# Performance work log

Measured on AMD Instinct MI355X. Metric: run time of the kernel, lower is better.

The kernel has to match this reference:

```python
import jax, jax.numpy as jnp
import numpy as np

D_MODEL = 1024
N_HEAD = 16

def setup_inputs() -> dict:
    key = jax.random.key(0)
    ks = jax.random.split(key, 11)
    B, S, D = 2, 2048, D_MODEL
    s = 1.0 / np.sqrt(D)
    inp = {
        'q': jax.random.normal(ks[0], (B, S, D), jnp.float32),
        'k': jax.random.normal(ks[1], (B, S, D), jnp.float32),
        'v': jax.random.normal(ks[2], (B, S, D), jnp.float32),
        'w_q': jax.random.normal(ks[3], (D, D), jnp.float32) * s,
        'b_q': jnp.zeros((D,), jnp.float32),
        'w_k': jax.random.normal(ks[4], (D, D), jnp.float32) * s,
        'b_k': jnp.zeros((D,), jnp.float32),
        'w_v': jax.random.normal(ks[5], (D, D), jnp.float32) * s,
        'b_v': jnp.zeros((D,), jnp.float32),
        'w_o': jax.random.normal(ks[6], (D, D), jnp.float32) * s,
        'b_o': jnp.zeros((D,), jnp.float32),
    }
    return inp

def _split_heads(x):
    B, S, D = x.shape
    return x.reshape(B, S, N_HEAD, D // N_HEAD).transpose(0, 2, 1, 3)  # [B,H,S,d]

def reference(q, k, v, w_q, b_q, w_k, b_k, w_v, b_v, w_o, b_o):
    # Linear projections (torch Linear: x @ W.T + b)
    qh = _split_heads(q @ w_q.T + b_q)
    kh = _split_heads(k @ w_k.T + b_k)
    vh = _split_heads(v @ w_v.T + b_v)
    d_k = qh.shape[-1]
    scores = jnp.einsum('bhqd,bhkd->bhqk', qh, kh) / jnp.sqrt(jnp.float32(d_k))
    attn = jax.nn.softmax(scores, axis=-1)
    out = jnp.einsum('bhqk,bhkd->bhqd', attn, vh)  # [B,H,S,d]
    B, H, S, d = out.shape
    out = out.transpose(0, 2, 1, 3).reshape(B, S, H * d)
    return out @ w_o.T + b_o
```

## Files before the change

### kernel.cpp

```cpp
#include <hip/hip_runtime.h>
#include <hip/hip_bf16.h>

typedef __hip_bfloat16 bf16;
typedef short bf16x8 __attribute__((ext_vector_type(8)));
typedef float f32x4 __attribute__((ext_vector_type(4)));

#define D_MODEL 1024
#define SEQ     2048
#define NHEAD   16
#define DHEAD   64
#define BATCH   2
#define MROWS   (BATCH*SEQ)
#define LOG2E   1.4426950408889634f

__device__ __forceinline__ void lds_dma16(const bf16* g, bf16* l) {
  __builtin_amdgcn_global_load_lds(
      (const __attribute__((address_space(1))) void*)g,
      (__attribute__((address_space(3))) void*)l, 16, 0, 0);
}

__device__ __forceinline__ uint4 pack8_f32(const float4 x0, const float4 x1) {
  union { uint4 q; bf16 h[8]; } pk;
  pk.h[0]=__float2bfloat16(x0.x); pk.h[1]=__float2bfloat16(x0.y);
  pk.h[2]=__float2bfloat16(x0.z); pk.h[3]=__float2bfloat16(x0.w);
  pk.h[4]=__float2bfloat16(x1.x); pk.h[5]=__float2bfloat16(x1.y);
  pk.h[6]=__float2bfloat16(x1.z); pk.h[7]=__float2bfloat16(x1.w);
  return pk.q;
}

__global__ __launch_bounds__(256) void convert7(
    const float* s0, const float* s1, const float* s2, const float* s3,
    const float* s4, const float* s5, const float* s6,
    bf16* d0, bf16* d1, bf16* d2, bf16* d3, bf16* d4, bf16* d5, bf16* d6)
{
  const float* S[7] = {s0,s1,s2,s3,s4,s5,s6};
  bf16*        D[7] = {d0,d1,d2,d3,d4,d5,d6};
  const int z = blockIdx.y;
  const int n8 = (z < 3) ? (MROWS*D_MODEL/8) : (D_MODEL*D_MODEL/8);
  for (int i = blockIdx.x*256 + threadIdx.x; i < n8; i += 512*256) {
    float4 a = ((const float4*)S[z])[2*i];
    float4 b = ((const float4*)S[z])[2*i+1];
    ((uint4*)D[z])[i] = pack8_f32(a, b);
  }
}

__global__ __launch_bounds__(256) void gemm3_dma(
    const bf16* A0, const bf16* A1, const bf16* A2,
    const bf16* W0, const bf16* W1, const bf16* W2,
    const float* B0, const float* B1, const float* B2,
    bf16* C0, bf16* C1, bf16* VpT)
{
  __shared__ __align__(16) bf16 As[8*128*8];
  __shared__ __align__(16) bf16 Ws[8*128*8];
  const int z = blockIdx.z;
  const bf16* A = (z == 0) ? A0 : (z == 1) ? A1 : A2;
  const bf16* W = (z == 0) ? W0 : (z == 1) ? W1 : W2;
  const float* Bv = (z == 0) ? B0 : (z == 1) ? B1 : B2;
  const int K = D_MODEL, N = D_MODEL;
  const int tid  = threadIdx.x;
  const int lane = tid & 63, wave = tid >> 6;
  const int wm   = wave >> 1, wn = wave & 1;
  const int quad = lane >> 4, l16 = lane & 15;
  const int row0 = blockIdx.y * 128, col0 = blockIdx.x * 128;

  const f32x4 zero = {0.f, 0.f, 0.f, 0.f};
  f32x4 acc[4][4];
  #pragma unroll
  for (int i = 0; i < 4; ++i)
    #pragma unroll
    for (int j = 0; j < 4; ++j) acc[i][j] = zero;

  for (int k0 = 0; k0 < K; k0 += 64) {
    __syncthreads();
    #pragma unroll
    for (int t = 0; t < 4; ++t) {
      int s = t*256 + tid;
      int g = s >> 7, r = s & 127;
      lds_dma16(A + (size_t)(row0 + r)*K + k0 + g*8, &As[s*8]);
      lds_dma16(W + (size_t)(col0 + r)*K + k0 + g*8, &Ws[s*8]);
    }
    __syncthreads();
    #pragma unroll
    for (int ks = 0; ks < 2; ++ks) {
      bf16x8 af[4], wf[4];
      #pragma unroll
      for (int mt = 0; mt < 4; ++mt)
        af[mt] = *(const bf16x8*)&As[((ks*4 + quad)*128 + wm*64 + mt*16 + l16)*8];
      #pragma unroll
      for (int nt = 0; nt < 4; ++nt)
        wf[nt] = *(const bf16x8*)&Ws[((ks*4 + quad)*128 + wn*64 + nt*16 + l16)*8];
      #pragma unroll
      for (int mt = 0; mt < 4; ++mt)
        #pragma unroll
        for (int nt = 0; nt < 4; ++nt)
          acc[mt][nt] = __builtin_amdgcn_mfma_f32_16x16x32_bf16(af[mt], wf[nt], acc[mt][nt], 0, 0, 0);
    }
  }

  if (z < 2) {
    bf16* C = (z == 0) ? C0 : C1;
    const float scale = (z == 0) ? 0.125f*LOG2E : 1.0f;
    #pragma unroll
    for (int nt = 0; nt < 4; ++nt) {
      int c = col0 + wn*64 + nt*16 + l16;
      float bv = Bv[c];
      #pragma unroll
      for (int mt = 0; mt < 4; ++mt) {
        int r = row0 + wm*64 + mt*16 + quad*4;
        #pragma unroll
        for (int j = 0; j < 4; ++j)
          C[(size_t)(r + j)*N + c] = __float2bfloat16((acc[mt][nt][j] + bv) * scale);
      }
    }
  } else {
    const int bb = row0 >> 11;
    const int sbase = (row0 & 2047) + wm*64;
    #pragma unroll
    for (int nt = 0; nt < 4; ++nt) {
      int c = col0 + wn*64 + nt*16 + l16;
      float bv = Bv[c];
      bf16* col = VpT + (size_t)((bb << 10) + c) * SEQ;
      #pragma unroll
      for (int mt = 0; mt < 4; ++mt) {
        int s = sbase + mt*16 + quad*4;
        union { uint2 u; bf16 h[4]; } pk;
        #pragma unroll
        for (int j = 0; j < 4; ++j) pk.h[j] = __float2bfloat16(acc[mt][nt][j] + bv);
        *(uint2*)(col + s) = pk.u;
      }
    }
  }
}

__global__ __launch_bounds__(256) void gemm_out_dma(
    const bf16* __restrict__ A, const bf16* __restrict__ W,
    const float* __restrict__ Bv, float* __restrict__ C)
{
  __shared__ __align__(16) bf16 As[8*128*8];
  __shared__ __align__(16) bf16 Ws[8*64*8];
  const int K = D_MODEL, N = D_MODEL;
  const int tid  = threadIdx.x;
  const int lane = tid & 63, wave = tid >> 6;
  const int wm   = wave >> 1, wn = wave & 1;
  const int quad = lane >> 4, l16 = lane & 15;
  const int row0 = blockIdx.y * 128, col0 = blockIdx.x * 64;

  const f32x4 zero = {0.f, 0.f, 0.f, 0.f};
  f32x4 acc[4][2];
  #pragma unroll
  for (int i = 0; i < 4; ++i)
    #pragma unroll
    for (int j = 0; j < 2; ++j) acc[i][j] = zero;

  for (int k0 = 0; k0 < K; k0 += 64) {
    __syncthreads();
    #pragma unroll
    for (int t = 0; t < 4; ++t) {
      int s = t*256 + tid;
      int g = s >> 7, r = s & 127;
      lds_dma16(A + (size_t)(row0 + r)*K + k0 + g*8, &As[s*8]);
    }
    #pragma unroll
    for (int t = 0; t < 2; ++t) {
      int s = t*256 + tid;
      int g = s >> 6, r = s & 63;
      lds_dma16(W + (size_t)(col0 + r)*K + k0 + g*8, &Ws[s*8]);
    }
    __syncthreads();
    #pragma unroll
    for (int ks = 0; ks < 2; ++ks) {
      bf16x8 af[4], wf[2];
      #pragma unroll
      for (int mt = 0; mt < 4; ++mt)
        af[mt] = *(const bf16x8*)&As[((ks*4 + quad)*128 + wm*64 + mt*16 + l16)*8];
      #pragma unroll
      for (int nt = 0; nt < 2; ++nt)
        wf[nt] = *(const bf16x8*)&Ws[((ks*4 + quad)*64 + wn*32 + nt*16 + l16)*8];
      #pragma unroll
      for (int mt = 0; mt < 4; ++mt)
        #pragma unroll
        for (int nt = 0; nt < 2; ++nt)
          acc[mt][nt] = __builtin_amdgcn_mfma_f32_16x16x32_bf16(af[mt], wf[nt], acc[mt][nt], 0, 0, 0);
    }
  }

  #pragma unroll
  for (int nt = 0; nt < 2; ++nt) {
    int c = col0 + wn*32 + nt*16 + l16;
    float bv = Bv[c];
    #pragma unroll
    for (int mt = 0; mt < 4; ++mt) {
      int r = row0 + wm*64 + mt*16 + quad*4;
      #pragma unroll
      for (int j = 0; j < 4; ++j)
        C[(size_t)(r + j)*N + c] = acc[mt][nt][j] + bv;
    }
  }
}

__global__ __launch_bounds__(256) void gemm3_fused(
    const float* A0, const float* A1, const float* A2,
    const float* W0, const float* W1, const float* W2,
    const float* B0, const float* B1, const float* B2,
    bf16* C0, bf16* C1, bf16* VpT)
{
  __shared__ __align__(16) bf16 As[4*128*8];
  __shared__ __align__(16) bf16 Ws[4*128*8];
  const int z = blockIdx.z;
  const float* A = (z == 0) ? A0 : (z == 1) ? A1 : A2;
  const float* W = (z == 0) ? W0 : (z == 1) ? W1 : W2;
  const float* Bv = (z == 0) ? B0 : (z == 1) ? B1 : B2;
  const int K = D_MODEL, N = D_MODEL;
  const int tid  = threadIdx.x;
  const int lane = tid & 63, wave = tid >> 6;
  const int wm   = wave >> 1, wn = wave & 1;
  const int quad = lane >> 4, l16 = lane & 15;
  const int row0 = blockIdx.y * 128, col0 = blockIdx.x * 128;

  const f32x4 zero = {0.f, 0.f, 0.f, 0.f};
  f32x4 acc[4][4];
  #pragma unroll
  for (int i = 0; i < 4; ++i)
    #pragma unroll
    for (int j = 0; j < 4; ++j) acc[i][j] = zero;

  for (int k0 = 0; k0 < K; k0 += 32) {
    __syncthreads();
    #pragma unroll
    for (int t = 0; t < 2; ++t) {
      int s = t*256 + tid;
      int g = s >> 7, r = s & 127;
      const float* Af = A + (size_t)(row0 + r)*K + k0 + g*8;
      *(uint4*)&As[s*8] = pack8_f32(((const float4*)Af)[0], ((const float4*)Af)[1]);
      const float* Wf = W + (size_t)(col0 + r)*K + k0 + g*8;
      *(uint4*)&Ws[s*8] = pack8_f32(((const float4*)Wf)[0], ((const float4*)Wf)[1]);
    }
    __syncthreads();
    bf16x8 af[4], wf[4];
    #pragma unroll
    for (int mt = 0; mt < 4; ++mt)
      af[mt] = *(const bf16x8*)&As[(quad*128 + wm*64 + mt*16 + l16)*8];
    #pragma unroll
    for (int nt = 0; nt < 4; ++nt)
      wf[nt] = *(const bf16x8*)&Ws[(quad*128 + wn*64 + nt*16 + l16)*8];
    #pragma unroll
    for (int mt = 0; mt < 4; ++mt)
      #pragma unroll
      for (int nt = 0; nt < 4; ++nt)
        acc[mt][nt] = __builtin_amdgcn_mfma_f32_16x16x32_bf16(af[mt], wf[nt], acc[mt][nt], 0, 0, 0);
  }

  if (z < 2) {
    bf16* C = (z == 0) ? C0 : C1;
    const float scale = (z == 0) ? 0.125f*LOG2E : 1.0f;
    #pragma unroll
    for (int nt = 0; nt < 4; ++nt) {
      int c = col0 + wn*64 + nt*16 + l16;
      float bv = Bv[c];
      #pragma unroll
      for (int mt = 0; mt < 4; ++mt) {
        int r = row0 + wm*64 + mt*16 + quad*4;
        #pragma unroll
        for (int j = 0; j < 4; ++j)
          C[(size_t)(r + j)*N + c] = __float2bfloat16((acc[mt][nt][j] + bv) * scale);
      }
    }
  } else {
    const int bb = row0 >> 11;
    const int sbase = (row0 & 2047) + wm*64;
    #pragma unroll
    for (int nt = 0; nt < 4; ++nt) {
      int c = col0 + wn*64 + nt*16 + l16;
      float bv = Bv[c];
      bf16* col = VpT + (size_t)((bb << 10) + c) * SEQ;
      #pragma unroll
      for (int mt = 0; mt < 4; ++mt) {
        int s = sbase + mt*16 + quad*4;
        union { uint2 u; bf16 h[4]; } pk;
        #pragma unroll
        for (int j = 0; j < 4; ++j) pk.h[j] = __float2bfloat16(acc[mt][nt][j] + bv);
        *(uint2*)(col + s) = pk.u;
      }
    }
  }
}

__global__ __launch_bounds__(256) void gemm_out_fused(
    const bf16* __restrict__ A, const float* __restrict__ W,
    const float* __restrict__ Bv, float* __restrict__ C)
{
  __shared__ __align__(16) bf16 As[4*128*8];
  __shared__ __align__(16) bf16 Ws[4*64*8];
  const int K = D_MODEL, N = D_MODEL;
  const int tid  = threadIdx.x;
  const int lane = tid & 63, wave = tid >> 6;
  const int wm   = wave >> 1, wn = wave & 1;
  const int quad = lane >> 4, l16 = lane & 15;
  const int row0 = blockIdx.y * 128, col0 = blockIdx.x * 64;

  const f32x4 zero = {0.f, 0.f, 0.f, 0.f};
  f32x4 acc[4][2];
  #pragma unroll
  for (int i = 0; i < 4; ++i)
    #pragma unroll
    for (int j = 0; j < 2; ++j) acc[i][j] = zero;

  for (int k0 = 0; k0 < K; k0 += 32) {
    __syncthreads();
    #pragma unroll
    for (int t = 0; t < 2; ++t) {
      int s = t*256 + tid;
      int g = s >> 7, r = s & 127;
      *(uint4*)&As[s*8] = *(const uint4*)(A + (size_t)(row0 + r)*K + k0 + g*8);
    }
    {
      int g = tid >> 6, r = tid & 63;
      const float* Wf = W + (size_t)(col0 + r)*K + k0 + g*8;
      *(uint4*)&Ws[tid*8] = pack8_f32(((const float4*)Wf)[0], ((const float4*)Wf)[1]);
    }
    __syncthreads();
    bf16x8 af[4], wf[2];
    #pragma unroll
    for (int mt = 0; mt < 4; ++mt)
      af[mt] = *(const bf16x8*)&As[(quad*128 + wm*64 + mt*16 + l16)*8];
    #pragma unroll
    for (int nt = 0; nt < 2; ++nt)
      wf[nt] = *(const bf16x8*)&Ws[(quad*64 + wn*32 + nt*16 + l16)*8];
    #pragma unroll
    for (int mt = 0; mt < 4; ++mt)
      #pragma unroll
      for (int nt = 0; nt < 2; ++nt)
        acc[mt][nt] = __builtin_amdgcn_mfma_f32_16x16x32_bf16(af[mt], wf[nt], acc[mt][nt], 0, 0, 0);
  }
  #pragma unroll
  for (int nt = 0; nt < 2; ++nt) {
    int c = col0 + wn*32 + nt*16 + l16;
    float bv = Bv[c];
    #pragma unroll
    for (int mt = 0; mt < 4; ++mt) {
      int r = row0 + wm*64 + mt*16 + quad*4;
      #pragma unroll
      for (int j = 0; j < 4; ++j)
        C[(size_t)(r + j)*N + c] = acc[mt][nt][j] + bv;
    }
  }
}

__global__ __launch_bounds__(512) void attn_fused(
    const bf16* __restrict__ Qp, const bf16* __restrict__ Kp,
    const bf16* __restrict__ VpT, bf16* __restrict__ Ao)
{
  __shared__ __align__(16) bf16 UN[128*128];
  __shared__ __align__(16) bf16 Ks[8*128*8];
  __shared__ __align__(16) bf16 Vt[64*16*8];

  const int tid  = threadIdx.x;
  const int lane = tid & 63, wave = tid >> 6;
  const int quad = lane >> 4, l16 = lane & 15;
  const int qt = blockIdx.x, h = blockIdx.y, b = blockIdx.z;
  const int q0 = qt * 128;
  const bf16* Qb = Qp + ((size_t)b*SEQ + q0)*D_MODEL + h*DHEAD;
  const bf16* Kb = Kp + (size_t)b*SEQ*D_MODEL + h*DHEAD;
  const bf16* Vg = VpT + (size_t)((b << 10) + h*DHEAD) * SEQ;

  #pragma unroll
  for (int t = 0; t < 2; ++t) {
    int s = t*512 + tid;
    int g = s >> 7, r = s & 127;
    lds_dma16(Qb + (size_t)r*D_MODEL + g*8, &UN[s*8]);
  }
  __syncthreads();

  const int wq0 = wave * 16;
  const int q   = wq0 + l16;
  bf16x8 qa[2];
  #pragma unroll
  for (int ks = 0; ks < 2; ++ks)
    qa[ks] = *(const bf16x8*)&UN[((ks*4 + quad)*128 + q)*8];
  __syncthreads();
  bf16* Ps = UN;
  const int swz = (l16 & 7) << 1;

  const f32x4 zero = {0.f, 0.f, 0.f, 0.f};
  f32x4 acc_o[4];
  #pragma unroll
  for (int dt = 0; dt < 4; ++dt) acc_o[dt] = zero;
  float m_s = -1e30f, l_s = 0.f;

  for (int kt = 0; kt < SEQ/128; ++kt) {
    #pragma unroll
    for (int t = 0; t < 2; ++t) {
      int s = t*512 + tid;
      int g = s >> 7, kk = s & 127;
      lds_dma16(Kb + (size_t)(kt*128 + kk)*D_MODEL + g*8, &Ks[s*8]);
    }
    #pragma unroll
    for (int t = 0; t < 2; ++t) {
      int c = t*512 + tid;
      int n = c >> 4, gk = c & 15;
      uint4 raw = *(const uint4*)(Vg + (size_t)n*SEQ + kt*128 + gk*8);
      int sw = (gk + n + (n >> 3)) & 15;
      *(uint4*)&Vt[(n*16 + sw)*8] = raw;
    }
    __syncthreads();

    f32x4 sc[8];
    #pragma unroll
    for (int kt2 = 0; kt2 < 8; ++kt2) sc[kt2] = zero;
    #pragma unroll
    for (int ks = 0; ks < 2; ++ks) {
      bf16x8 kf[8];
      #pragma unroll
      for (int kt2 = 0; kt2 < 8; ++kt2)
        kf[kt2] = *(const bf16x8*)&Ks[((ks*4 + quad)*128 + kt2*16 + l16)*8];
      #pragma unroll
      for (int kt2 = 0; kt2 < 8; ++kt2)
        sc[kt2] = __builtin_amdgcn_mfma_f32_16x16x32_bf16(kf[kt2], qa[ks], sc[kt2], 0, 0, 0);
    }

    float vmax = -1e30f;
    #pragma unroll
    for (int kt2 = 0; kt2 < 8; ++kt2) {
      f32x4 s4 = sc[kt2];
      vmax = fmaxf(vmax, fmaxf(fmaxf(s4[0], s4[1]), fmaxf(s4[2], s4[3])));
    }
    vmax = fmaxf(vmax, __shfl_xor(vmax, 16));
    vmax = fmaxf(vmax, __shfl_xor(vmax, 32));
    float mnew  = fmaxf(m_s, vmax);
    float alpha = __builtin_amdgcn_exp2f(m_s - mnew);
    float rs = 0.f;
    #pragma unroll
    for (int kt2 = 0; kt2 < 8; ++kt2) {
      float p0 = __builtin_amdgcn_exp2f(sc[kt2][0] - mnew);
      float p1 = __builtin_amdgcn_exp2f(sc[kt2][1] - mnew);
      float p2 = __builtin_amdgcn_exp2f(sc[kt2][2] - mnew);
      float p3 = __builtin_amdgcn_exp2f(sc[kt2][3] - mnew);
      rs += (p0 + p1) + (p2 + p3);
      union { uint2 u; bf16 hh[4]; } pk;
      pk.hh[0] = __float2bfloat16(p0); pk.hh[1] = __float2bfloat16(p1);
      pk.hh[2] = __float2bfloat16(p2); pk.hh[3] = __float2bfloat16(p3);
      int phys = (kt2*4 + quad) ^ swz;
      *(uint2*)&Ps[q*128 + phys*4] = pk.u;
    }
    rs += __shfl_xor(rs, 16);
    rs += __shfl_xor(rs, 32);
    l_s = l_s*alpha + rs;
    m_s = mnew;
    #pragma unroll
    for (int dt = 0; dt < 4; ++dt) acc_o[dt] = acc_o[dt] * alpha;

    #pragma unroll
    for (int ks2 = 0; ks2 < 4; ++ks2) {
      bf16x8 vf[4], pa;
      #pragma unroll
      for (int dt = 0; dt < 4; ++dt) {
        int n = dt*16 + l16;
        int sw = (ks2*4 + quad + n + (n >> 3)) & 15;
        vf[dt] = *(const bf16x8*)&Vt[(n*16 + sw)*8];
      }
      int phys = (ks2*8 + quad*2) ^ swz;
      pa = *(const bf16x8*)&Ps[q*128 + phys*4];
      #pragma unroll
      for (int dt = 0; dt < 4; ++dt)
        acc_o[dt] = __builtin_amdgcn_mfma_f32_16x16x32_bf16(vf[dt], pa, acc_o[dt], 0, 0, 0);
    }
    __syncthreads();
  }

  bf16* Ob = Ao + ((size_t)b*SEQ + q0)*D_MODEL + h*DHEAD;
  float inv = 1.f / l_s;
  #pragma unroll
  for (int dt = 0; dt < 4; ++dt) {
    union { uint2 u; bf16 hh[4]; } pk;
    #pragma unroll
    for (int j = 0; j < 4; ++j) pk.hh[j] = __float2bfloat16(acc_o[dt][j] * inv);
    *(uint2*)(Ob + (size_t)q*D_MODEL + dt*16 + quad*4) = pk.u;
  }
}

extern "C" void kernel_launch(void* const* d_in, const int* in_sizes, int n_in,
                              void* d_out, int out_size, void* d_ws, size_t ws_size,
                              hipStream_t stream) {
  const float* q   = (const float*)d_in[0];
  const float* k   = (const float*)d_in[1];
  const float* v   = (const float*)d_in[2];
  const float* w_q = (const float*)d_in[3];
  const float* b_q = (const float*)d_in[4];
  const float* w_k = (const float*)d_in[5];
  const float* b_k = (const float*)d_in[6];
  const float* w_v = (const float*)d_in[7];
  const float* b_v = (const float*)d_in[8];
  const float* w_o = (const float*)d_in[9];
  const float* b_o = (const float*)d_in[10];

  const size_t nbuf = (size_t)MROWS * D_MODEL;
  const size_t wbuf = (size_t)D_MODEL * D_MODEL;
  bf16* Kp  = (bf16*)d_out;
  bf16* VpT = Kp + nbuf;

  const size_t needA = 256 + (3*nbuf + 4*wbuf + nbuf) * 2;
  if (ws_size >= needA) {
    bf16* qc  = (bf16*)((char*)d_ws + 256);
    bf16* kc  = qc  + nbuf;
    bf16* vc  = kc  + nbuf;
    bf16* wqc = vc  + nbuf;
    bf16* wkc = wqc + wbuf;
    bf16* wvc = wkc + wbuf;
    bf16* woc = wvc + wbuf;
    bf16* Qp  = woc + wbuf;
    bf16* Ao  = Qp;

    convert7<<<dim3(512,7), 256, 0, stream>>>(q, k, v, w_q, w_k, w_v, w_o,
                                              qc, kc, vc, wqc, wkc, wvc, woc);
    gemm3_dma<<<dim3(8,32,3), 256, 0, stream>>>(qc, kc, vc, wqc, wkc, wvc,
                                                b_q, b_k, b_v, Qp, Kp, VpT);
    attn_fused<<<dim3(16,16,2), 512, 0, stream>>>(Qp, Kp, VpT, Ao);
    gemm_out_dma<<<dim3(16,32), 256, 0, stream>>>(Ao, woc, b_o, (float*)d_out);
  } else {
    bf16* Qp = (bf16*)((char*)d_ws + 256);
    bf16* Ao = Qp;
    gemm3_fused<<<dim3(8,32,3), 256, 0, stream>>>(q, k, v, w_q, w_k, w_v,
                                                  b_q, b_k, b_v, Qp, Kp, VpT);
    attn_fused<<<dim3(16,16,2), 512, 0, stream>>>(Qp, Kp, VpT, Ao);
    gemm_out_fused<<<dim3(16,32), 256, 0, stream>>>(Ao, w_o, b_o, (float*)d_out);
  }
}
```

Before: 309.7 us.

## Swap MFMA operands for vectorized GEMM stores and prefetch V tiles in attention

In the projection GEMMs, the MFMA operands are swapped so each lane holds four consecutive output columns. This lets the epilogue write packed 8-byte bf16 or 16-byte float4 stores and read the bias with float4 loads, instead of scalar strided stores. In the attention kernel, the V-transpose tile for the next iteration is loaded from global memory into registers one step ahead, and the end-of-loop barrier moves to the top of the loop. This hides global load latency behind compute, at the cost of extra registers and an altered synchronization pattern.

```diff
diff --git a/kernel.cpp b/kernel.cpp
--- a/kernel.cpp
+++ b/kernel.cpp
@@ -56,6 +56,7 @@
   const bf16* A = (z == 0) ? A0 : (z == 1) ? A1 : A2;
   const bf16* W = (z == 0) ? W0 : (z == 1) ? W1 : W2;
   const float* Bv = (z == 0) ? B0 : (z == 1) ? B1 : B2;
+  const bool swapped = (z < 2);
   const int K = D_MODEL, N = D_MODEL;
   const int tid  = threadIdx.x;
   const int lane = tid & 63, wave = tid >> 6;
@@ -89,27 +90,38 @@
       #pragma unroll
       for (int nt = 0; nt < 4; ++nt)
         wf[nt] = *(const bf16x8*)&Ws[((ks*4 + quad)*128 + wn*64 + nt*16 + l16)*8];
-      #pragma unroll
-      for (int mt = 0; mt < 4; ++mt)
-        #pragma unroll
-        for (int nt = 0; nt < 4; ++nt)
-          acc[mt][nt] = __builtin_amdgcn_mfma_f32_16x16x32_bf16(af[mt], wf[nt], acc[mt][nt], 0, 0, 0);
-    }
-  }
-
-  if (z < 2) {
+      if (swapped) {
+        #pragma unroll
+        for (int mt = 0; mt < 4; ++mt)
+          #pragma unroll
+          for (int nt = 0; nt < 4; ++nt)
+            acc[mt][nt] = __builtin_amdgcn_mfma_f32_16x16x32_bf16(wf[nt], af[mt], acc[mt][nt], 0, 0, 0);
+      } else {
+        #pragma unroll
+        for (int mt = 0; mt < 4; ++mt)
+          #pragma unroll
+          for (int nt = 0; nt < 4; ++nt)
+            acc[mt][nt] = __builtin_amdgcn_mfma_f32_16x16x32_bf16(af[mt], wf[nt], acc[mt][nt], 0, 0, 0);
+      }
+    }
+  }
+
+  if (swapped) {
     bf16* C = (z == 0) ? C0 : C1;
     const float scale = (z == 0) ? 0.125f*LOG2E : 1.0f;
     #pragma unroll
-    for (int nt = 0; nt < 4; ++nt) {
-      int c = col0 + wn*64 + nt*16 + l16;
-      float bv = Bv[c];
-      #pragma unroll
-      for (int mt = 0; mt < 4; ++mt) {
-        int r = row0 + wm*64 + mt*16 + quad*4;
-        #pragma unroll
-        for (int j = 0; j < 4; ++j)
-          C[(size_t)(r + j)*N + c] = __float2bfloat16((acc[mt][nt][j] + bv) * scale);
+    for (int mt = 0; mt < 4; ++mt) {
+      int r = row0 + wm*64 + mt*16 + l16;
+      #pragma unroll
+      for (int nt = 0; nt < 4; ++nt) {
+        int c0 = col0 + wn*64 + nt*16 + quad*4;
+        float4 b4 = *(const float4*)(Bv + c0);
+        union { uint2 u; bf16 h[4]; } pk;
+        pk.h[0] = __float2bfloat16((acc[mt][nt][0] + b4.x) * scale);
+        pk.h[1] = __float2bfloat16((acc[mt][nt][1] + b4.y) * scale);
+        pk.h[2] = __float2bfloat16((acc[mt][nt][2] + b4.z) * scale);
+        pk.h[3] = __float2bfloat16((acc[mt][nt][3] + b4.w) * scale);
+        *(uint2*)&C[(size_t)r*N + c0] = pk.u;
       }
     }
   } else {
@@ -180,20 +192,21 @@
       for (int mt = 0; mt < 4; ++mt)
         #pragma unroll
         for (int nt = 0; nt < 2; ++nt)
-          acc[mt][nt] = __builtin_amdgcn_mfma_f32_16x16x32_bf16(af[mt], wf[nt], acc[mt][nt], 0, 0, 0);
-    }
-  }
-
-  #pragma unroll
-  for (int nt = 0; nt < 2; ++nt) {
-    int c = col0 + wn*32 + nt*16 + l16;
-    float bv = Bv[c];
-    #pragma unroll
-    for (int mt = 0; mt < 4; ++mt) {
-      int r = row0 + wm*64 + mt*16 + quad*4;
-      #pragma unroll
-      for (int j = 0; j < 4; ++j)
-        C[(size_t)(r + j)*N + c] = acc[mt][nt][j] + bv;
+          acc[mt][nt] = __builtin_amdgcn_mfma_f32_16x16x32_bf16(wf[nt], af[mt], acc[mt][nt], 0, 0, 0);
+    }
+  }
+
+  #pragma unroll
+  for (int mt = 0; mt < 4; ++mt) {
+    int r = row0 + wm*64 + mt*16 + l16;
+    #pragma unroll
+    for (int nt = 0; nt < 2; ++nt) {
+      int c0 = col0 + wn*32 + nt*16 + quad*4;
+      float4 b4 = *(const float4*)(Bv + c0);
+      float4 o;
+      o.x = acc[mt][nt][0] + b4.x; o.y = acc[mt][nt][1] + b4.y;
+      o.z = acc[mt][nt][2] + b4.z; o.w = acc[mt][nt][3] + b4.w;
+      *(float4*)&C[(size_t)r*N + c0] = o;
     }
   }
 }
@@ -210,6 +223,7 @@
   const float* A = (z == 0) ? A0 : (z == 1) ? A1 : A2;
   const float* W = (z == 0) ? W0 : (z == 1) ? W1 : W2;
   const float* Bv = (z == 0) ? B0 : (z == 1) ? B1 : B2;
+  const bool swapped = (z < 2);
   const int K = D_MODEL, N = D_MODEL;
   const int tid  = threadIdx.x;
   const int lane = tid & 63, wave = tid >> 6;
@@ -243,26 +257,37 @@
     #pragma unroll
     for (int nt = 0; nt < 4; ++nt)
       wf[nt] = *(const bf16x8*)&Ws[(quad*128 + wn*64 + nt*16 + l16)*8];
-    #pragma unroll
-    for (int mt = 0; mt < 4; ++mt)
-      #pragma unroll
-      for (int nt = 0; nt < 4; ++nt)
-        acc[mt][nt] = __builtin_amdgcn_mfma_f32_16x16x32_bf16(af[mt], wf[nt], acc[mt][nt], 0, 0, 0);
-  }
-
-  if (z < 2) {
+    if (swapped) {
+      #pragma unroll
+      for (int mt = 0; mt < 4; ++mt)
+        #pragma unroll
+        for (int nt = 0; nt < 4; ++nt)
+          acc[mt][nt] = __builtin_amdgcn_mfma_f32_16x16x32_bf16(wf[nt], af[mt], acc[mt][nt], 0, 0, 0);
+    } else {
+      #pragma unroll
+      for (int mt = 0; mt < 4; ++mt)
+        #pragma unroll
+        for (int nt = 0; nt < 4; ++nt)
+          acc[mt][nt] = __builtin_amdgcn_mfma_f32_16x16x32_bf16(af[mt], wf[nt], acc[mt][nt], 0, 0, 0);
+    }
+  }
+
+  if (swapped) {
     bf16* C = (z == 0) ? C0 : C1;
     const float scale = (z == 0) ? 0.125f*LOG2E : 1.0f;
     #pragma unroll
-    for (int nt = 0; nt < 4; ++nt) {
-      int c = col0 + wn*64 + nt*16 + l16;
-      float bv = Bv[c];
-      #pragma unroll
-      for (int mt = 0; mt < 4; ++mt) {
-        int r = row0 + wm*64 + mt*16 + quad*4;
-        #pragma unroll
-        for (int j = 0; j < 4; ++j)
-          C[(size_t)(r + j)*N + c] = __float2bfloat16((acc[mt][nt][j] + bv) * scale);
+    for (int mt = 0; mt < 4; ++mt) {
+      int r = row0 + wm*64 + mt*16 + l16;
+      #pragma unroll
+      for (int nt = 0; nt < 4; ++nt) {
+        int c0 = col0 + wn*64 + nt*16 + quad*4;
+        float4 b4 = *(const float4*)(Bv + c0);
+        union { uint2 u; bf16 h[4]; } pk;
+        pk.h[0] = __float2bfloat16((acc[mt][nt][0] + b4.x) * scale);
+        pk.h[1] = __float2bfloat16((acc[mt][nt][1] + b4.y) * scale);
+        pk.h[2] = __float2bfloat16((acc[mt][nt][2] + b4.z) * scale);
+        pk.h[3] = __float2bfloat16((acc[mt][nt][3] + b4.w) * scale);
+        *(uint2*)&C[(size_t)r*N + c0] = pk.u;
       }
     }
   } else {
@@ -330,18 +355,19 @@
     for (int mt = 0; mt < 4; ++mt)
       #pragma unroll
       for (int nt = 0; nt < 2; ++nt)
-        acc[mt][nt] = __builtin_amdgcn_mfma_f32_16x16x32_bf16(af[mt], wf[nt], acc[mt][nt], 0, 0, 0);
-  }
-  #pragma unroll
-  for (int nt = 0; nt < 2; ++nt) {
-    int c = col0 + wn*32 + nt*16 + l16;
-    float bv = Bv[c];
-    #pragma unroll
-    for (int mt = 0; mt < 4; ++mt) {
-      int r = row0 + wm*64 + mt*16 + quad*4;
-      #pragma unroll
-      for (int j = 0; j < 4; ++j)
-        C[(size_t)(r + j)*N + c] = acc[mt][nt][j] + bv;
+        acc[mt][nt] = __builtin_amdgcn_mfma_f32_16x16x32_bf16(wf[nt], af[mt], acc[mt][nt], 0, 0, 0);
+  }
+  #pragma unroll
+  for (int mt = 0; mt < 4; ++mt) {
+    int r = row0 + wm*64 + mt*16 + l16;
+    #pragma unroll
+    for (int nt = 0; nt < 2; ++nt) {
+      int c0 = col0 + wn*32 + nt*16 + quad*4;
+      float4 b4 = *(const float4*)(Bv + c0);
+      float4 o;
+      o.x = acc[mt][nt][0] + b4.x; o.y = acc[mt][nt][1] + b4.y;
+      o.z = acc[mt][nt][2] + b4.z; o.w = acc[mt][nt][3] + b4.w;
+      *(float4*)&C[(size_t)r*N + c0] = o;
     }
   }
 }
@@ -377,10 +403,16 @@
   #pragma unroll
   for (int ks = 0; ks < 2; ++ks)
     qa[ks] = *(const bf16x8*)&UN[((ks*4 + quad)*128 + q)*8];
-  __syncthreads();
   bf16* Ps = UN;
   const int swz = (l16 & 7) << 1;
 
+  const int vn0 = tid >> 4,        vgk0 = tid & 15;
+  const int vn1 = (512+tid) >> 4,  vgk1 = (512+tid) & 15;
+  const int vsw0 = (vgk0 + vn0 + (vn0 >> 3)) & 15;
+  const int vsw1 = (vgk1 + vn1 + (vn1 >> 3)) & 15;
+  uint4 vreg0 = *(const uint4*)(Vg + (size_t)vn0*SEQ + vgk0*8);
+  uint4 vreg1 = *(const uint4*)(Vg + (size_t)vn1*SEQ + vgk1*8);
+
   const f32x4 zero = {0.f, 0.f, 0.f, 0.f};
   f32x4 acc_o[4];
   #pragma unroll
@@ -388,19 +420,19 @@
   float m_s = -1e30f, l_s = 0.f;
 
   for (int kt = 0; kt < SEQ/128; ++kt) {
+    __syncthreads();
     #pragma unroll
     for (int t = 0; t < 2; ++t) {
       int s = t*512 + tid;
       int g = s >> 7, kk = s & 127;
       lds_dma16(Kb + (size_t)(kt*128 + kk)*D_MODEL + g*8, &Ks[s*8]);
     }
-    #pragma unroll
-    for (int t = 0; t < 2; ++t) {
-      int c = t*512 + tid;
-      int n = c >> 4, gk = c & 15;
-      uint4 raw = *(const uint4*)(Vg + (size_t)n*SEQ + kt*128 + gk*8);
-      int sw = (gk + n + (n >> 3)) & 15;
-      *(uint4*)&Vt[(n*16 + sw)*8] = raw;
+    *(uint4*)&Vt[(vn0*16 + vsw0)*8] = vreg0;
+    *(uint4*)&Vt[(vn1*16 + vsw1)*8] = vreg1;
+    {
+      int ktn = (kt + 1 < SEQ/128) ? kt + 1 : kt;
+      vreg0 = *(const uint4*)(Vg + (size_t)vn0*SEQ + ktn*128 + vgk0*8);
+      vreg1 = *(const uint4*)(Vg + (size_t)vn1*SEQ + ktn*128 + vgk1*8);
     }
     __syncthreads();
 
@@ -464,7 +496,6 @@
       for (int dt = 0; dt < 4; ++dt)
         acc_o[dt] = __builtin_amdgcn_mfma_f32_16x16x32_bf16(vf[dt], pa, acc_o[dt], 0, 0, 0);
     }
-    __syncthreads();
   }
 
   bf16* Ob = Ao + ((size_t)b*SEQ + q0)*D_MODEL + h*DHEAD;
```

After: 307.0 us. No clear change (-0.9%).
